# Optimization experiments

Hardware: AMD Instinct MI355X
Metric: run time of the kernel (lower is better)

The kernel has to match this reference:

```python
import jax, jax.numpy as jnp
import numpy as np

# Locally-connected 2D convolution (torch legacy SpatialConvolutionLocal)
# out[b,o,h,w] = sum_{c,i,j} weight[h,w,o,c,i,j] * x_pad[b,c,h*dH+i,w*dW+j] + bias[o,h,w]

B, CIN, IH, IW = 32, 32, 64, 64
COUT, KH, KW = 64, 3, 3
DH, DW = 1, 1
PADH, PADW = 1, 1
OH = (IH + 2 * PADH - KH) // DH + 1
OW = (IW + 2 * PADW - KW) // DW + 1


def setup_inputs() -> dict:
    key = jax.random.key(0)
    k1, k2, k3 = jax.random.split(key, 3)
    stdv = 1.0 / np.sqrt(KW * KH * CIN)
    x = jax.random.normal(k1, (B, CIN, IH, IW), dtype=jnp.float32)
    weight = jax.random.uniform(k2, (OH, OW, COUT, CIN, KH, KW), dtype=jnp.float32,
                                minval=-stdv, maxval=stdv)
    bias = jax.random.uniform(k3, (COUT, OH, OW), dtype=jnp.float32,
                              minval=-stdv, maxval=stdv)
    return {"x": x, "weight": weight, "bias": bias}


def _extract_patches(x):
    # x: [B, C, IH, IW] -> patches [B, C, KH, KW, OH, OW]
    xp = jnp.pad(x, ((0, 0), (0, 0), (PADH, PADH), (PADW, PADW)))
    rows = []
    for i in range(KH):  # small fixed kernel loop (9 iters), not a data-dim loop
        cols = []
        for j in range(KW):
            cols.append(xp[:, :, i:i + OH * DH:DH, j:j + OW * DW:DW])
        rows.append(jnp.stack(cols, axis=2))  # [B, C, KW, OH, OW]
    return jnp.stack(rows, axis=2)  # [B, C, KH, KW, OH, OW]


def reference(x, weight, bias):
    patches = _extract_patches(x)  # [B, C, KH, KW, OH, OW]
    # per-position GEMM: distinct weight matrix at each (h, w)
    out = jnp.einsum('bcijhw,hwocij->bohw', patches, weight)
    return out + bias[None]  # [B, COUT, OH, OW]
```

## Files before the change

kernel.cpp:

```cpp
#include <hip/hip_runtime.h>


#define KP 88

typedef __attribute__((ext_vector_type(8))) short short8;
typedef __attribute__((ext_vector_type(16))) float f32x16;

__device__ __forceinline__ unsigned f2bf(float f) {
    unsigned u = __builtin_bit_cast(unsigned, f);
    return (u + 0x7FFFu + ((u >> 16) & 1u)) >> 16;
}

__global__ __launch_bounds__(256, 3) void lcconv_kernel(
    const float* __restrict__ xg,
    const float* __restrict__ wg,
    const float* __restrict__ bg,
    float* __restrict__ outg)
{
    __shared__ unsigned short Wl[4 * 32 * KP];
    __shared__ unsigned short Pl[4 * 32 * KP];

    const int tid = threadIdx.x;
    const int bid = blockIdx.x;
    const int oh = bid & 1;
    const int ws = (bid >> 1) & 15;
    const int h  = bid >> 5;
    const int w0 = ws * 4;
    const int og = oh * 32;

    {
        unsigned short* base = (tid & 128) ? Pl : Wl;
        int row = tid & 127;
        *(short8*)(base + row * KP + 72) = (short8)0;
    }

    f32x16 acc;
#pragma unroll
    for (int i = 0; i < 16; i++) acc[i] = 0.f;

    const int lane = tid & 63;
    const int wv   = tid >> 6;
    const int mrow = lane & 31;
    const int g    = lane >> 5;

    float4 wreg[9];
    float2 xreg[12];

#pragma unroll
    for (int it = 0; it < 9; it++) {
        int f4 = it * 256 + tid;
        int run = f4 / 18, within = f4 - run * 18;
        int p = run >> 5, o = run & 31;
        wreg[it] = *(const float4*)(
            wg + ((h * 64 + (w0 + p)) * 64 + og + o) * 288 + within * 4);
    }
#pragma unroll
    for (int it = 0; it < 12; it++) {
        int task = it * 256 + tid;
        int f2i = task & 3, row = task >> 2;
        int b = row / 24, rem = row - b * 24;
        int c = rem / 3, y3 = rem - c * 3;
        int y = h + y3 - 1;
        int gx0 = w0 - 2 + 2 * f2i;
        if ((unsigned)y < 64u && (unsigned)gx0 < 64u)
            xreg[it] = *(const float2*)(xg + ((b * 32 + c) * 64 + y) * 64 + gx0);
        else
            xreg[it] = float2{0.f, 0.f};
    }

    for (int cc = 0; cc < 4; cc++) {
        __syncthreads();

#pragma unroll
        for (int it = 0; it < 9; it++) {
            int f4 = it * 256 + tid;
            int run = f4 / 18, within = f4 - run * 18;
            float4 w4 = wreg[it];
            unsigned long long pk = (unsigned long long)f2bf(w4.x)
                | ((unsigned long long)f2bf(w4.y) << 16)
                | ((unsigned long long)f2bf(w4.z) << 32)
                | ((unsigned long long)f2bf(w4.w) << 48);
            *(unsigned long long*)(Wl + run * KP + within * 4) = pk;
        }

#pragma unroll
        for (int it = 0; it < 12; it++) {
            int task = it * 256 + tid;
            int f2i = task & 3, row = task >> 2;
            int b = row / 24, rem = row - b * 24;
            int c = rem / 3, y3 = rem - c * 3;
            int kb = c * 9 + y3 * 3;
            int pb = b * KP + kb;
            unsigned bx0 = f2bf(xreg[it].x);
            unsigned bx1 = f2bf(xreg[it].y);
#pragma unroll
            for (int q = 0; q < 2; q++) {
                int xc = f2i * 2 + q;
                unsigned short bv = (unsigned short)(q ? bx1 : bx0);
#pragma unroll
                for (int j = 0; j < 3; j++) {
                    int p = xc - 1 - j;
                    if ((unsigned)p < 4u)
                        Pl[p * (32 * KP) + pb + j] = bv;
                }
            }
        }
        __syncthreads();

        if (cc < 3) {
            const int c0n = (cc + 1) * 8;
#pragma unroll
            for (int it = 0; it < 9; it++) {
                int f4 = it * 256 + tid;
                int run = f4 / 18, within = f4 - run * 18;
                int p = run >> 5, o = run & 31;
                wreg[it] = *(const float4*)(
                    wg + ((h * 64 + (w0 + p)) * 64 + og + o) * 288 + c0n * 9 + within * 4);
            }
#pragma unroll
            for (int it = 0; it < 12; it++) {
                int task = it * 256 + tid;
                int f2i = task & 3, row = task >> 2;
                int b = row / 24, rem = row - b * 24;
                int c = rem / 3, y3 = rem - c * 3;
                int y = h + y3 - 1;
                int gx0 = w0 - 2 + 2 * f2i;
                if ((unsigned)y < 64u && (unsigned)gx0 < 64u)
                    xreg[it] = *(const float2*)(xg + ((b * 32 + c0n + c) * 64 + y) * 64 + gx0);
                else
                    xreg[it] = float2{0.f, 0.f};
            }
        }

#pragma unroll
        for (int ks = 0; ks < 5; ks++) {
            short8 a  = *(const short8*)(Pl + (wv * 32 + mrow) * KP + ks * 16 + g * 8);
            short8 b8 = *(const short8*)(Wl + (wv * 32 + mrow) * KP + ks * 16 + g * 8);
            acc = __builtin_amdgcn_mfma_f32_32x32x16_bf16(a, b8, acc, 0, 0, 0);
        }
    }
    __syncthreads();

    float* outl = (float*)Wl;
#pragma unroll
    for (int r = 0; r < 16; r++) {
        int row = (r & 3) + 8 * (r >> 2) + 4 * g;
        outl[(wv * 32 + row) * 32 + mrow] = acc[r];
    }
    __syncthreads();

#pragma unroll
    for (int it = 0; it < 4; it++) {
        int id = it * 256 + tid;
        int b = id >> 5;
        int o = id & 31;
        float4 v;
        v.x = outl[0 * 1024 + b * 32 + o];
        v.y = outl[1 * 1024 + b * 32 + o];
        v.z = outl[2 * 1024 + b * 32 + o];
        v.w = outl[3 * 1024 + b * 32 + o];
        const float4 bb = *(const float4*)(bg + ((og + o) * 64 + h) * 64 + w0);
        v.x += bb.x; v.y += bb.y; v.z += bb.z; v.w += bb.w;
        *(float4*)(outg + ((b * 64 + og + o) * 64 + h) * 64 + w0) = v;
    }
}

extern "C" void kernel_launch(void* const* d_in, const int* in_sizes, int n_in,
                              void* d_out, int out_size, void* d_ws, size_t ws_size,
                              hipStream_t stream) {
    const float* x = (const float*)d_in[0];
    const float* w = (const float*)d_in[1];
    const float* b = (const float*)d_in[2];
    float* out = (float*)d_out;
    lcconv_kernel<<<dim3(2048), dim3(256), 0, stream>>>(x, w, b, out);
}
```

Measured before the change: 508.8 us.

## Stream weights directly into MFMA operands and stage one shared input halo tile

The kernel no longer stages weights through shared memory. Each lane loads its own weight fragment straight from global memory with nontemporal loads and converts it to bf16 in registers. The input is loaded once per block as a bf16 halo tile with a channel rotation to reduce bank conflicts, and the A operand is gathered from it through index arithmetic. This removes the 4-stage loop and its barriers, and the block index is remapped for XCD locality with a higher occupancy hint. The cost is scalar LDS gathers per MFMA, and weight load latency is now exposed in the inner loop.

```diff
diff --git a/kernel.cpp b/kernel.cpp
--- a/kernel.cpp
+++ b/kernel.cpp
@@ -1,151 +1,106 @@
 #include <hip/hip_runtime.h>
 
 
-#define KP 88
-
 typedef __attribute__((ext_vector_type(8))) short short8;
 typedef __attribute__((ext_vector_type(16))) float f32x16;
+typedef __attribute__((ext_vector_type(4))) float f32x4;
 
 __device__ __forceinline__ unsigned f2bf(float f) {
     unsigned u = __builtin_bit_cast(unsigned, f);
     return (u + 0x7FFFu + ((u >> 16) & 1u)) >> 16;
 }
 
-__global__ __launch_bounds__(256, 3) void lcconv_kernel(
+__global__ __launch_bounds__(256, 4) void lcconv_kernel(
     const float* __restrict__ xg,
     const float* __restrict__ wg,
     const float* __restrict__ bg,
     float* __restrict__ outg)
 {
-    __shared__ unsigned short Wl[4 * 32 * KP];
-    __shared__ unsigned short Pl[4 * 32 * KP];
+    __shared__ unsigned short Xl[32 * 32 * 3 * 6];
 
-    const int tid = threadIdx.x;
-    const int bid = blockIdx.x;
-    const int oh = bid & 1;
-    const int ws = (bid >> 1) & 15;
-    const int h  = bid >> 5;
-    const int w0 = ws * 4;
-    const int og = oh * 32;
+    const int tid  = threadIdx.x;
+    const int B    = blockIdx.x;
+    const int xcd  = B & 7;
+    const int slot = B >> 3;
+    const int wm   = slot & 7;
+    const int gi   = xcd * 32 + (slot >> 3);
+    const int h    = gi >> 2;
+    const int wq2  = (gi >> 1) & 1;
+    const int oh   = gi & 1;
+    const int w0   = wq2 * 32 + wm * 4;
+    const int og   = oh * 32;
 
-    {
-        unsigned short* base = (tid & 128) ? Pl : Wl;
-        int row = tid & 127;
-        *(short8*)(base + row * KP + 72) = (short8)0;
+#pragma unroll
+    for (int t = 0; t < 12; t++) {
+        int task = t * 256 + tid;
+        int b   = task / 96;
+        int rem = task - b * 96;
+        int c   = rem / 3;
+        int y3  = rem - c * 3;
+        int y   = h + y3 - 1;
+        float v0 = 0.f, v1 = 0.f, v2 = 0.f, v3 = 0.f, v4 = 0.f, v5 = 0.f;
+        if ((unsigned)y < 64u) {
+            const float* row = xg + ((b * 32 + c) * 64 + y) * 64;
+            float4 m = *(const float4*)(row + w0);
+            v1 = m.x; v2 = m.y; v3 = m.z; v4 = m.w;
+            if (w0 > 0)      v0 = row[w0 - 1];
+            if (w0 + 4 < 64) v5 = row[w0 + 4];
+        }
+        int cr = (c + b) & 31;
+        unsigned* dst = (unsigned*)(Xl + ((b * 32 + cr) * 3 + y3) * 6);
+        dst[0] = f2bf(v0) | (f2bf(v1) << 16);
+        dst[1] = f2bf(v2) | (f2bf(v3) << 16);
+        dst[2] = f2bf(v4) | (f2bf(v5) << 16);
     }
+    __syncthreads();
+
+    const int lane = tid & 63;
+    const int wv   = tid >> 6;
+    const int n    = lane & 31;
+    const int g    = lane >> 5;
+
+    const float* wbase = wg
+        + (((h * 64) + (w0 + wv)) * 64 + og + n) * 288 + g * 8;
 
     f32x16 acc;
 #pragma unroll
     for (int i = 0; i < 16; i++) acc[i] = 0.f;
 
-    const int lane = tid & 63;
-    const int wv   = tid >> 6;
-    const int mrow = lane & 31;
-    const int g    = lane >> 5;
-
-    float4 wreg[9];
-    float2 xreg[12];
+    const int abase = n * 576 + wv;
 
 #pragma unroll
-    for (int it = 0; it < 9; it++) {
-        int f4 = it * 256 + tid;
-        int run = f4 / 18, within = f4 - run * 18;
-        int p = run >> 5, o = run & 31;
-        wreg[it] = *(const float4*)(
-            wg + ((h * 64 + (w0 + p)) * 64 + og + o) * 288 + within * 4);
-    }
+    for (int ks = 0; ks < 18; ks++) {
+        f32x4 wa = __builtin_nontemporal_load((const f32x4*)(wbase + ks * 16));
+        f32x4 wb = __builtin_nontemporal_load((const f32x4*)(wbase + ks * 16 + 4));
+
+        short8 a;
+        int k0 = ks * 16 + g * 8;
 #pragma unroll
-    for (int it = 0; it < 12; it++) {
-        int task = it * 256 + tid;
-        int f2i = task & 3, row = task >> 2;
-        int b = row / 24, rem = row - b * 24;
-        int c = rem / 3, y3 = rem - c * 3;
-        int y = h + y3 - 1;
-        int gx0 = w0 - 2 + 2 * f2i;
-        if ((unsigned)y < 64u && (unsigned)gx0 < 64u)
-            xreg[it] = *(const float2*)(xg + ((b * 32 + c) * 64 + y) * 64 + gx0);
-        else
-            xreg[it] = float2{0.f, 0.f};
+        for (int e = 0; e < 8; e++) {
+            int k = k0 + e;
+            int c = (k * 456) >> 12;
+            int t = k - c * 9;
+            int i = (t * 11) >> 5;
+            int j = t - i * 3;
+            int cr = (c + n) & 31;
+            a[e] = (short)Xl[abase + cr * 18 + i * 6 + j];
+        }
+
+        short8 w8;
+        w8[0] = (short)f2bf(wa[0]); w8[1] = (short)f2bf(wa[1]);
+        w8[2] = (short)f2bf(wa[2]); w8[3] = (short)f2bf(wa[3]);
+        w8[4] = (short)f2bf(wb[0]); w8[5] = (short)f2bf(wb[1]);
+        w8[6] = (short)f2bf(wb[2]); w8[7] = (short)f2bf(wb[3]);
+
+        acc = __builtin_amdgcn_mfma_f32_32x32x16_bf16(a, w8, acc, 0, 0, 0);
     }
 
-    for (int cc = 0; cc < 4; cc++) {
-        __syncthreads();
-
-#pragma unroll
-        for (int it = 0; it < 9; it++) {
-            int f4 = it * 256 + tid;
-            int run = f4 / 18, within = f4 - run * 18;
-            float4 w4 = wreg[it];
-            unsigned long long pk = (unsigned long long)f2bf(w4.x)
-                | ((unsigned long long)f2bf(w4.y) << 16)
-                | ((unsigned long long)f2bf(w4.z) << 32)
-                | ((unsigned long long)f2bf(w4.w) << 48);
-            *(unsigned long long*)(Wl + run * KP + within * 4) = pk;
-        }
-
-#pragma unroll
-        for (int it = 0; it < 12; it++) {
-            int task = it * 256 + tid;
-            int f2i = task & 3, row = task >> 2;
-            int b = row / 24, rem = row - b * 24;
-            int c = rem / 3, y3 = rem - c * 3;
-            int kb = c * 9 + y3 * 3;
-            int pb = b * KP + kb;
-            unsigned bx0 = f2bf(xreg[it].x);
-            unsigned bx1 = f2bf(xreg[it].y);
-#pragma unroll
-            for (int q = 0; q < 2; q++) {
-                int xc = f2i * 2 + q;
-                unsigned short bv = (unsigned short)(q ? bx1 : bx0);
-#pragma unroll
-                for (int j = 0; j < 3; j++) {
-                    int p = xc - 1 - j;
-                    if ((unsigned)p < 4u)
-                        Pl[p * (32 * KP) + pb + j] = bv;
-                }
-            }
-        }
-        __syncthreads();
-
-        if (cc < 3) {
-            const int c0n = (cc + 1) * 8;
-#pragma unroll
-            for (int it = 0; it < 9; it++) {
-                int f4 = it * 256 + tid;
-                int run = f4 / 18, within = f4 - run * 18;
-                int p = run >> 5, o = run & 31;
-                wreg[it] = *(const float4*)(
-                    wg + ((h * 64 + (w0 + p)) * 64 + og + o) * 288 + c0n * 9 + within * 4);
-            }
-#pragma unroll
-            for (int it = 0; it < 12; it++) {
-                int task = it * 256 + tid;
-                int f2i = task & 3, row = task >> 2;
-                int b = row / 24, rem = row - b * 24;
-                int c = rem / 3, y3 = rem - c * 3;
-                int y = h + y3 - 1;
-                int gx0 = w0 - 2 + 2 * f2i;
-                if ((unsigned)y < 64u && (unsigned)gx0 < 64u)
-                    xreg[it] = *(const float2*)(xg + ((b * 32 + c0n + c) * 64 + y) * 64 + gx0);
-                else
-                    xreg[it] = float2{0.f, 0.f};
-            }
-        }
-
-#pragma unroll
-        for (int ks = 0; ks < 5; ks++) {
-            short8 a  = *(const short8*)(Pl + (wv * 32 + mrow) * KP + ks * 16 + g * 8);
-            short8 b8 = *(const short8*)(Wl + (wv * 32 + mrow) * KP + ks * 16 + g * 8);
-            acc = __builtin_amdgcn_mfma_f32_32x32x16_bf16(a, b8, acc, 0, 0, 0);
-        }
-    }
     __syncthreads();
-
-    float* outl = (float*)Wl;
+    float* outl = (float*)Xl;
 #pragma unroll
     for (int r = 0; r < 16; r++) {
         int row = (r & 3) + 8 * (r >> 2) + 4 * g;
-        outl[(wv * 32 + row) * 32 + mrow] = acc[r];
+        outl[(wv * 32 + row) * 32 + n] = acc[r];
     }
     __syncthreads();
 
```

New measurement: 536.4 us. +5.4%, slower.
